# Performance work log

Measured on AMD Instinct MI355X. Metric: run time of the kernel, lower is better.

Reference implementation:

```python
import jax, jax.numpy as jnp
import numpy as np

B, D, N, MSRC, H = 4, 256, 2048, 2048, 4
DIM = D // H  # per-head dim = 64
EPS = 1e-3


def _conv1x1(W, b, z):
    # 1x1 Conv1d == per-position linear: W [out,in], z [B,in,N]
    return jnp.einsum('oc,bcn->bon', W, z) + b[None, :, None]


def setup_inputs() -> dict:
    key = jax.random.key(0)
    ks = jax.random.split(key, 20)
    s = 0.05
    x = jax.random.normal(ks[0], (B, D, N), dtype=jnp.float32)
    source = jax.random.normal(ks[1], (B, D, MSRC), dtype=jnp.float32)
    mask = (jax.random.uniform(ks[2], (B, N, MSRC)) > 0.3).astype(jnp.float32)
    Wq = jax.random.normal(ks[3], (D, D), jnp.float32) * s
    bq = jax.random.normal(ks[4], (D,), jnp.float32) * s
    Wk = jax.random.normal(ks[5], (D, D), jnp.float32) * s
    bk = jax.random.normal(ks[6], (D,), jnp.float32) * s
    Wv = jax.random.normal(ks[7], (D, D), jnp.float32) * s
    bv = jax.random.normal(ks[8], (D,), jnp.float32) * s
    Wm = jax.random.normal(ks[9], (D, D), jnp.float32) * s
    bm = jax.random.normal(ks[10], (D,), jnp.float32) * s
    W1 = jax.random.normal(ks[11], (2 * D, 2 * D), jnp.float32) * s
    b1 = jax.random.normal(ks[12], (2 * D,), jnp.float32) * s
    gamma = jnp.ones((2 * D,), jnp.float32)
    beta = jnp.zeros((2 * D,), jnp.float32)
    rmean = jax.random.normal(ks[13], (2 * D,), jnp.float32) * 0.1
    rvar = jax.random.uniform(ks[14], (2 * D,), jnp.float32) + 0.5
    W2 = jax.random.normal(ks[15], (D, 2 * D), jnp.float32) * s
    b2 = jnp.zeros((D,), jnp.float32)  # nn.init.constant_(mlp[-1].bias, 0.0)
    return dict(x=x, source=source, mask=mask, Wq=Wq, bq=bq, Wk=Wk, bk=bk,
                Wv=Wv, bv=bv, Wm=Wm, bm=bm, W1=W1, b1=b1, gamma=gamma,
                beta=beta, rmean=rmean, rvar=rvar, W2=W2, b2=b2)


def reference(x, source, mask, Wq, bq, Wk, bk, Wv, bv, Wm, bm,
              W1, b1, gamma, beta, rmean, rvar, W2, b2):
    b = x.shape[0]
    # channel dim split as (dim, heads) per torch .view(B, dim, H, -1)
    q = _conv1x1(Wq, bq, x).reshape(b, DIM, H, -1)        # [B,d,H,N]
    k = _conv1x1(Wk, bk, source).reshape(b, DIM, H, -1)   # [B,d,H,M]
    v = _conv1x1(Wv, bv, source).reshape(b, DIM, H, -1)   # [B,d,H,M]
    scores = jnp.einsum('bdhn,bdhm->bhnm', q, k) / (DIM ** 0.5)
    neg = -jnp.finfo(scores.dtype).max
    scores = jnp.where(mask[:, None, :, :] > 0, scores, neg)
    prob = jax.nn.softmax(scores, axis=-1)                # [B,H,N,M]
    msg = jnp.einsum('bhnm,bdhm->bdhn', prob, v).reshape(b, D, -1)
    message = _conv1x1(Wm, bm, msg)                       # [B,D,N]
    y = jnp.concatenate([x, message], axis=1)             # [B,2D,N]
    h = _conv1x1(W1, b1, y)
    # BatchNorm1d (eval mode, eps=1e-3)
    h = (h - rmean[None, :, None]) * jax.lax.rsqrt(rvar + EPS)[None, :, None]
    h = h * gamma[None, :, None] + beta[None, :, None]
    h = jax.nn.relu(h)
    return _conv1x1(W2, b2, h)                            # [B,D,N]
```

## Files before the change

kernel.cpp:

```cpp
#include <hip/hip_runtime.h>

constexpr int Bb = 4;
constexpr int Dd = 256;
constexpr int Nn = 2048;
constexpr int Mm = 2048;
constexpr int Hh = 4;
constexpr int D2 = 512;
constexpr int NT = Bb * Nn;

#define FMAXV 3.402823466e38f

typedef _Float16 half8 __attribute__((ext_vector_type(8)));
typedef _Float16 half4v __attribute__((ext_vector_type(4)));
typedef float f32x4 __attribute__((ext_vector_type(4)));

typedef const __attribute__((address_space(1))) void* gas_p;
typedef __attribute__((address_space(3))) void* las_p;

__device__ __forceinline__ void gload16(const void* g, void* l) {
    __builtin_amdgcn_global_load_lds((gas_p)g, (las_p)l, 16, 0, 0);
}

__global__ __launch_bounds__(256)
void prep_all_kernel(const float* __restrict__ Wq, const float* __restrict__ bq,
                     const float* __restrict__ Wk, const float* __restrict__ bk,
                     const float* __restrict__ Wv, const float* __restrict__ bv,
                     const float* __restrict__ Wm,
                     const float* __restrict__ W1, const float* __restrict__ b1,
                     const float* __restrict__ gamma, const float* __restrict__ beta,
                     const float* __restrict__ rmean, const float* __restrict__ rvar,
                     const float* __restrict__ W2, const float* __restrict__ mask,
                     const float* __restrict__ x, const float* __restrict__ source,
                     _Float16* __restrict__ Wqp, float* __restrict__ bqp,
                     _Float16* __restrict__ Wkvp, float* __restrict__ bkvp,
                     _Float16* __restrict__ Wmp,
                     _Float16* __restrict__ W1p, float* __restrict__ b1f,
                     _Float16* __restrict__ W2p,
                     unsigned long long* __restrict__ bmask,
                     _Float16* __restrict__ Yp, _Float16* __restrict__ Sp) {
    const int r = blockIdx.x, t = threadIdx.x;
    if (r < 256) {
        const int h = r >> 6, d = r & 63, so = d * Hh + h;
        Wqp[r * 256 + t] = (_Float16)Wq[so * 256 + t];
        if (t == 0) bqp[r] = bq[so];
    } else if (r < 768) {
        const int rr = r - 256, part = rr >> 8, o = rr & 255;
        const int h = o >> 6, d = o & 63, so = d * Hh + h;
        const float* Ws = part ? Wv : Wk;
        const float* bs = part ? bv : bk;
        Wkvp[rr * 256 + t] = (_Float16)Ws[so * 256 + t];
        if (t == 0) bkvp[rr] = bs[so];
    } else if (r < 1024) {
        const int o = r - 768;
        const int h = t >> 6, d = t & 63, sk = d * Hh + h;
        Wmp[o * 256 + t] = (_Float16)Wm[o * 256 + sk];
    } else if (r < 1536) {
        const int o = r - 1024;
        const float s = gamma[o] * rsqrtf(rvar[o] + 1e-3f);
        W1p[o * 512 + t]       = (_Float16)(W1[o * 512 + t] * s);
        W1p[o * 512 + t + 256] = (_Float16)(W1[o * 512 + t + 256] * s);
        if (t == 0) b1f[o] = (b1[o] - rmean[o]) * s + beta[o];
    } else if (r < 1792) {
        const int o = r - 1536;
        W2p[o * 512 + t]       = (_Float16)W2[o * 512 + t];
        W2p[o * 512 + t + 256] = (_Float16)W2[o * 512 + t + 256];
    } else if (r < 3840) {
        const int id = r - 1792;
        const int w = t >> 6, lane = t & 63;
        const int row = id * 4 + w;
        const float* mrow = mask + (size_t)row * Mm;
        unsigned long long* brow = bmask + (size_t)row * (Mm / 64);
        #pragma unroll 4
        for (int word = 0; word < Mm / 64; ++word) {
            const float v = mrow[word * 64 + lane];
            const unsigned long long bits = __ballot(v > 0.f);
            if (lane == 0) brow[word] = bits;
        }
    } else {
        __shared__ _Float16 Ts[64][72];
        const int px = r - 3840;
        const int n0 = (px & 31) * 64, c0 = ((px >> 5) & 3) * 64;
        const int z = px >> 7, b = z >> 1, which = z & 1;
        const float* src = which ? source : x;
        _Float16* dst = which ? Sp : Yp;
        const int stride = which ? 256 : 512;
        const int cl = t >> 2, np = (t & 3) * 16;
        const float* sp = src + ((size_t)b * Dd + c0 + cl) * Nn + n0 + np;
        #pragma unroll
        for (int i = 0; i < 4; ++i) {
            float4 v = *(const float4*)(sp + i * 4);
            Ts[np + i * 4 + 0][cl] = (_Float16)v.x;
            Ts[np + i * 4 + 1][cl] = (_Float16)v.y;
            Ts[np + i * 4 + 2][cl] = (_Float16)v.z;
            Ts[np + i * 4 + 3][cl] = (_Float16)v.w;
        }
        __syncthreads();
        const int nl = t >> 2, cp = (t & 3) * 16;
        half8 a0 = *(const half8*)&Ts[nl][cp];
        half8 a1 = *(const half8*)&Ts[nl][cp + 8];
        _Float16* dp = dst + ((size_t)b * Nn + n0 + nl) * stride + c0 + cp;
        *(half8*)dp = a0;
        *(half8*)(dp + 8) = a1;
    }
}

__global__ __launch_bounds__(256)
void gemm4w_kernel(const _Float16* __restrict__ A, const _Float16* __restrict__ A2,
                   const _Float16* __restrict__ W, const float* __restrict__ bias,
                   _Float16* __restrict__ dst0, _Float16* __restrict__ dst1,
                   _Float16* __restrict__ dst2, float* __restrict__ dstF,
                   int K, int sA, int sOut, int modeSel, int relu, float oscale) {
    __shared__ __align__(16) _Float16 As[2 * 128 * 64];
    __shared__ __align__(16) _Float16 Bs[2 * 64 * 64];
    __shared__ __align__(16) _Float16 Es[4][16][72];

    const int t = threadIdx.x;
    const int w = t >> 6, lane = t & 63, quad = lane >> 4, l16 = lane & 15;
    const int n0 = blockIdx.x * 128;
    const int og0 = blockIdx.y * 64;

    int mode = 0, oloc0 = og0;
    const _Float16* Ab = A;
    int sAl = sA;
    _Float16* d0 = dst0;
    float osc = oscale;
    if (modeSel == 3) {
        const int part = blockIdx.y >> 2;
        if (part == 1)      { Ab = A2; sAl = 256; d0 = dst1; oloc0 = og0 - 256; osc = 1.0f; }
        else if (part == 2) { Ab = A2; sAl = 256; mode = 1; oloc0 = og0 - 512; osc = 1.0f; }
    } else if (modeSel == 2) {
        mode = 2;
    }

    const int srow = t >> 3, sslot = t & 7;
    const int schunk = sslot ^ (srow & 7);

    f32x4 acc[2][4] = {};
    const int nk = K / 64;
    int buf = 0;

    {
        #pragma unroll
        for (int c = 0; c < 4; ++c)
            gload16(Ab + (size_t)(n0 + c * 32 + srow) * sAl + schunk * 8,
                    As + c * 2048 + t * 8);
        #pragma unroll
        for (int c = 0; c < 2; ++c)
            gload16(W + (size_t)(og0 + c * 32 + srow) * K + schunk * 8,
                    Bs + c * 2048 + t * 8);
        __asm__ volatile("s_waitcnt vmcnt(0)" ::: "memory");
        __syncthreads();
    }

    #pragma unroll 1
    for (int kt = 0; kt < nk; ++kt) {
        if (kt + 1 < nk) {
            const int k0 = (kt + 1) * 64, nb = buf ^ 1;
            #pragma unroll
            for (int c = 0; c < 4; ++c)
                gload16(Ab + (size_t)(n0 + c * 32 + srow) * sAl + k0 + schunk * 8,
                        As + nb * 8192 + c * 2048 + t * 8);
            #pragma unroll
            for (int c = 0; c < 2; ++c)
                gload16(W + (size_t)(og0 + c * 32 + srow) * K + k0 + schunk * 8,
                        Bs + nb * 4096 + c * 2048 + t * 8);
        }
        #pragma unroll
        for (int ks = 0; ks < 2; ++ks) {
            const int csw = ((ks * 4 + quad) ^ (l16 & 7)) * 8;
            half8 af[2], bf[4];
            #pragma unroll
            for (int i = 0; i < 2; ++i)
                af[i] = *(const half8*)&As[buf * 8192 + (w * 32 + i * 16 + l16) * 64 + csw];
            #pragma unroll
            for (int j = 0; j < 4; ++j)
                bf[j] = *(const half8*)&Bs[buf * 4096 + (j * 16 + l16) * 64 + csw];
            #pragma unroll
            for (int i = 0; i < 2; ++i)
                #pragma unroll
                for (int j = 0; j < 4; ++j)
                    acc[i][j] = __builtin_amdgcn_mfma_f32_16x16x32_f16(af[i], bf[j], acc[i][j], 0, 0, 0);
        }
        if (kt + 1 < nk) {
            __asm__ volatile("s_waitcnt vmcnt(0)" ::: "memory");
            __syncthreads();
            buf ^= 1;
        }
    }

    float bcol[4];
    #pragma unroll
    for (int j = 0; j < 4; ++j) bcol[j] = bias[og0 + j * 16 + l16];

    if (mode == 0) {
        #pragma unroll
        for (int i = 0; i < 2; ++i) {
            #pragma unroll
            for (int j = 0; j < 4; ++j)
                #pragma unroll
                for (int reg = 0; reg < 4; ++reg) {
                    float v = (acc[i][j][reg] + bcol[j]) * osc;
                    if (relu) v = fmaxf(v, 0.f);
                    Es[w][quad * 4 + reg][j * 16 + l16] = (_Float16)v;
                }
            __asm__ volatile("s_waitcnt lgkmcnt(0)" ::: "memory");
            const int row = lane & 15, oseg = (lane >> 4) * 16;
            half8 e0 = *(const half8*)&Es[w][row][oseg];
            half8 e1 = *(const half8*)&Es[w][row][oseg + 8];
            _Float16* dp = d0 + (size_t)(n0 + w * 32 + i * 16 + row) * sOut + oloc0 + oseg;
            *(half8*)dp = e0;
            *(half8*)(dp + 8) = e1;
            __asm__ volatile("s_waitcnt lgkmcnt(0)" ::: "memory");
        }
    } else if (mode == 1) {
        #pragma unroll
        for (int i = 0; i < 2; ++i) {
            const int ng = n0 + w * 32 + i * 16 + quad * 4;
            const int bidx = ng >> 11, m0 = ng & 2047;
            #pragma unroll
            for (int j = 0; j < 4; ++j) {
                const int o = oloc0 + j * 16 + l16;
                half4v pv;
                #pragma unroll
                for (int reg = 0; reg < 4; ++reg) pv[reg] = (_Float16)(acc[i][j][reg] + bcol[j]);
                *(half4v*)(dst2 + ((size_t)bidx * 256 + o) * (size_t)Mm + m0) = pv;
            }
        }
    } else {
        #pragma unroll
        for (int i = 0; i < 2; ++i) {
            const int ng = n0 + w * 32 + i * 16 + quad * 4;
            const int bidx = ng >> 11, m0 = ng & 2047;
            #pragma unroll
            for (int j = 0; j < 4; ++j) {
                const int o = og0 + j * 16 + l16;
                f32x4 v;
                #pragma unroll
                for (int reg = 0; reg < 4; ++reg) v[reg] = acc[i][j][reg] + bcol[j];
                *(f32x4*)(dstF + ((size_t)bidx * 256 + o) * (size_t)Nn + m0) = v;
            }
        }
    }
}

__global__ __launch_bounds__(256)
void attn_mfma_kernel(const _Float16* __restrict__ Qp, const _Float16* __restrict__ Kp,
                      const _Float16* __restrict__ Vt,
                      const unsigned int* __restrict__ bmask,
                      _Float16* __restrict__ Oa, _Float16* __restrict__ Ob,
                      float* __restrict__ La, float* __restrict__ Lb) {
    __shared__ __align__(16) _Float16 Ks[64][72];
    __shared__ __align__(16) _Float16 Vs[64][72];
    __shared__ __align__(16) _Float16 Ps[4][16][72];

    const int id = blockIdx.x;
    const int xcd = id & 7, loc = id >> 3;
    const int bh = xcd * 2 + (loc >> 6);
    const int sub = loc & 63;
    const int mhalf = sub & 1;
    const int n0 = (sub >> 1) * 64;
    const int b = bh >> 2, h = bh & 3;

    const int t = threadIdx.x;
    const int w = t >> 6, lane = t & 63, quad = lane >> 4, l16 = lane & 15;

    const _Float16* qp = Qp + ((size_t)b * Nn + n0 + w * 16 + l16) * 256 + h * 64 + quad * 8;
    const half8 qa0 = *(const half8*)(qp);
    const half8 qa1 = *(const half8*)(qp + 32);

    const _Float16* Kstg = Kp + (size_t)b * Nn * 256 + h * 64;
    const _Float16* Vstg = Vt + ((size_t)b * 256 + h * 64) * (size_t)Mm;
    const int sr = t >> 2, sc = (t & 3) * 16;

    const unsigned int* bmBase = bmask + ((size_t)b * Nn + n0 + w * 16 + quad * 4) * (Mm / 32);

    _Float16* Od = mhalf ? Ob : Oa;
    float* Ld = mhalf ? Lb : La;
    const int mbeg = mhalf * (Mm / 2);

    float lo[4] = {0.f, 0.f, 0.f, 0.f};
    f32x4 O[4] = {};

    half8 sk0, sk1, sv0, sv1;
    auto stage_load = [&](int m0) {
        const _Float16* ks = Kstg + (size_t)(m0 + sr) * 256 + sc;
        sk0 = *(const half8*)(ks);
        sk1 = *(const half8*)(ks + 8);
        const _Float16* vs = Vstg + (size_t)sr * Mm + m0 + sc;
        sv0 = *(const half8*)(vs);
        sv1 = *(const half8*)(vs + 8);
    };
    auto stage_write = [&]() {
        *(half8*)&Ks[sr][sc]     = sk0;
        *(half8*)&Ks[sr][sc + 8] = sk1;
        *(half8*)&Vs[sr][sc]     = sv0;
        *(half8*)&Vs[sr][sc + 8] = sv1;
    };

    stage_load(mbeg);
    stage_write();
    __syncthreads();

    #pragma unroll 1
    for (int it = 0; it < (Mm / 2) / 64; ++it) {
        const int m0 = mbeg + it * 64;
        if (it < (Mm / 2) / 64 - 1) stage_load(m0 + 64);

        uint2 bmv[4];
        #pragma unroll
        for (int reg = 0; reg < 4; ++reg)
            bmv[reg] = *(const uint2*)(bmBase + (size_t)reg * (Mm / 32) + (m0 >> 5));

        f32x4 S[4];
        #pragma unroll
        for (int mt = 0; mt < 4; ++mt) {
            half8 k0 = *(const half8*)&Ks[mt * 16 + l16][quad * 8];
            half8 k1 = *(const half8*)&Ks[mt * 16 + l16][32 + quad * 8];
            f32x4 z = {0.f, 0.f, 0.f, 0.f};
            z = __builtin_amdgcn_mfma_f32_16x16x32_f16(qa0, k0, z, 0, 0, 0);
            z = __builtin_amdgcn_mfma_f32_16x16x32_f16(qa1, k1, z, 0, 0, 0);
            S[mt] = z;
        }

        float p[4][4];
        #pragma unroll
        for (int reg = 0; reg < 4; ++reg) {
            const unsigned losh = bmv[reg].x >> l16;
            const unsigned hish = bmv[reg].y >> l16;
            p[0][reg] = (losh & 1u)         ? __expf(S[0][reg]) : 0.f;
            p[1][reg] = ((losh >> 16) & 1u) ? __expf(S[1][reg]) : 0.f;
            p[2][reg] = (hish & 1u)         ? __expf(S[2][reg]) : 0.f;
            p[3][reg] = ((hish >> 16) & 1u) ? __expf(S[3][reg]) : 0.f;
        }
        #pragma unroll
        for (int reg = 0; reg < 4; ++reg)
            lo[reg] += (p[0][reg] + p[1][reg]) + (p[2][reg] + p[3][reg]);

        #pragma unroll
        for (int mt = 0; mt < 4; ++mt)
            #pragma unroll
            for (int reg = 0; reg < 4; ++reg)
                Ps[w][quad * 4 + reg][mt * 16 + l16] = (_Float16)p[mt][reg];
        __asm__ volatile("s_waitcnt lgkmcnt(0)" ::: "memory");
        half8 pa0 = *(const half8*)&Ps[w][l16][quad * 8];
        half8 pa1 = *(const half8*)&Ps[w][l16][32 + quad * 8];

        #pragma unroll
        for (int dt = 0; dt < 4; ++dt) {
            half8 v0 = *(const half8*)&Vs[dt * 16 + l16][quad * 8];
            half8 v1 = *(const half8*)&Vs[dt * 16 + l16][32 + quad * 8];
            O[dt] = __builtin_amdgcn_mfma_f32_16x16x32_f16(pa0, v0, O[dt], 0, 0, 0);
            O[dt] = __builtin_amdgcn_mfma_f32_16x16x32_f16(pa1, v1, O[dt], 0, 0, 0);
        }

        if (it < (Mm / 2) / 64 - 1) {
            __syncthreads();
            stage_write();
            __syncthreads();
        }
    }

    #pragma unroll
    for (int reg = 0; reg < 4; ++reg) {
        float s = lo[reg];
        s += __shfl_xor(s, 1);
        s += __shfl_xor(s, 2);
        s += __shfl_xor(s, 4);
        s += __shfl_xor(s, 8);
        lo[reg] = s;
    }

    _Float16* op = Od + ((size_t)b * Nn + n0 + w * 16 + quad * 4) * 256 + h * 64 + l16;
    #pragma unroll
    for (int reg = 0; reg < 4; ++reg)
        #pragma unroll
        for (int dt = 0; dt < 4; ++dt)
            op[(size_t)reg * 256 + dt * 16] = (_Float16)(O[dt][reg] * 0.0625f);
    if (l16 == 0) {
        #pragma unroll
        for (int reg = 0; reg < 4; ++reg)
            Ld[((size_t)b * Nn + n0 + w * 16 + quad * 4 + reg) * 4 + h] = lo[reg] * 0.0625f;
    }
}

__global__ __launch_bounds__(256)
void combine_kernel(const _Float16* __restrict__ Oa, const _Float16* __restrict__ Ob,
                    const float* __restrict__ La, const float* __restrict__ Lb,
                    _Float16* __restrict__ out) {
    const int gid = blockIdx.x * 256 + threadIdx.x;
    const int row = gid >> 5, chunk = gid & 31;
    const int h = chunk >> 3;
    const float L = La[row * 4 + h] + Lb[row * 4 + h];
    const float inv = 1.0f / L;
    half8 a = *(const half8*)(Oa + (size_t)row * 256 + chunk * 8);
    half8 c = *(const half8*)(Ob + (size_t)row * 256 + chunk * 8);
    half8 o;
    #pragma unroll
    for (int k = 0; k < 8; ++k)
        o[k] = (_Float16)(((float)a[k] + (float)c[k]) * inv);
    *(half8*)(out + (size_t)row * 256 + chunk * 8) = o;
}

extern "C" void kernel_launch(void* const* d_in, const int* in_sizes, int n_in,
                              void* d_out, int out_size, void* d_ws, size_t ws_size,
                              hipStream_t stream) {
    const float* x      = (const float*)d_in[0];
    const float* source = (const float*)d_in[1];
    const float* mask   = (const float*)d_in[2];
    const float* Wq = (const float*)d_in[3];
    const float* bq = (const float*)d_in[4];
    const float* Wk = (const float*)d_in[5];
    const float* bk = (const float*)d_in[6];
    const float* Wv = (const float*)d_in[7];
    const float* bv = (const float*)d_in[8];
    const float* Wm = (const float*)d_in[9];
    const float* bm = (const float*)d_in[10];
    const float* W1 = (const float*)d_in[11];
    const float* b1 = (const float*)d_in[12];
    const float* gamma = (const float*)d_in[13];
    const float* beta  = (const float*)d_in[14];
    const float* rmean = (const float*)d_in[15];
    const float* rvar  = (const float*)d_in[16];
    const float* W2 = (const float*)d_in[17];
    const float* b2 = (const float*)d_in[18];
    float* outp = (float*)d_out;

    char* wsb = (char*)d_ws;
    _Float16* Yp   = (_Float16*)wsb;
    _Float16* Sp   = (_Float16*)(wsb + (8u << 20));
    _Float16* Qp   = (_Float16*)(wsb + (12u << 20));
    _Float16* Kp   = (_Float16*)(wsb + (16u << 20));
    _Float16* Vt   = (_Float16*)(wsb + (20u << 20));
    _Float16* msgp = (_Float16*)(wsb + (24u << 20));
    _Float16* Hp   = (_Float16*)(wsb + (28u << 20));
    unsigned long long* bmask = (unsigned long long*)(wsb + (28u << 20));
    _Float16* Ob = (_Float16*)(wsb + (30u << 20));
    float* La = (float*)(wsb + (34u << 20));
    float* Lb = (float*)(wsb + (34u << 20) + (128u << 10));
    char* wp = wsb + (36u << 20);
    _Float16* Wqp  = (_Float16*)wp;            wp += 256 * 256 * 2;
    _Float16* Wkvp = (_Float16*)wp;            wp += 512 * 256 * 2;
    _Float16* Wmp  = (_Float16*)wp;            wp += 256 * 256 * 2;
    _Float16* W1p  = (_Float16*)wp;            wp += 512 * 512 * 2;
    _Float16* W2p  = (_Float16*)wp;            wp += 256 * 512 * 2;
    float* bqp  = (float*)wp;                  wp += 256 * 4;
    float* bkvp = (float*)wp;                  wp += 512 * 4;
    float* b1f  = (float*)wp;                  wp += 512 * 4;

    prep_all_kernel<<<4864, 256, 0, stream>>>(
        Wq, bq, Wk, bk, Wv, bv, Wm, W1, b1, gamma, beta, rmean, rvar, W2, mask,
        x, source, Wqp, bqp, Wkvp, bkvp, Wmp, W1p, b1f, W2p, bmask, Yp, Sp);

    gemm4w_kernel<<<dim3(NT / 128, 12), 256, 0, stream>>>(
        Yp, Sp, Wqp, bqp, Qp, Kp, Vt, nullptr, 256, 512, 256, 3, 0, 0.125f);

    attn_mfma_kernel<<<1024, 256, 0, stream>>>(Qp, Kp, Vt,
                                               (const unsigned int*)bmask,
                                               msgp, Ob, La, Lb);

    combine_kernel<<<1024, 256, 0, stream>>>(msgp, Ob, La, Lb, Sp);

    gemm4w_kernel<<<dim3(NT / 128, 4), 256, 0, stream>>>(
        Sp, nullptr, Wmp, bm, Yp + 256, nullptr, nullptr, nullptr, 256, 256, 512, 0, 0, 1.0f);
    gemm4w_kernel<<<dim3(NT / 128, 8), 256, 0, stream>>>(
        Yp, nullptr, W1p, b1f, Hp, nullptr, nullptr, nullptr, 512, 512, 512, 0, 1, 1.0f);
    gemm4w_kernel<<<dim3(NT / 128, 4), 256, 0, stream>>>(
        Hp, nullptr, W2p, b2, nullptr, nullptr, nullptr, outp, 512, 512, 0, 2, 0, 1.0f);
}
```

Measured before the change: 237.7 us.

## Fuse attention combine, merge projection, and MLP into one kernel

Replaces the combine kernel and three separate GEMM launches with one kernel per 16-row tile. The tile merges the two attention halves, applies the Wm projection, W1 with ReLU, and W2, keeping intermediates in LDS so the msg and hidden activations never round-trip through global memory. Weights are read directly from global/L2 with no LDS staging. Only 512 blocks run and each uses a 16-row tile, so weight reuse per block is low and occupancy may be limited.

```diff
diff --git a/kernel.cpp b/kernel.cpp
--- a/kernel.cpp
+++ b/kernel.cpp
@@ -383,22 +383,126 @@
     }
 }
 
+template<int NJ>
+__device__ __forceinline__ void mm_stage(const _Float16* As, int sAl,
+                                         const _Float16* W, int K,
+                                         int oc0, int l16, int quad,
+                                         f32x4 (&acc)[NJ]) {
+    const _Float16* bRow[NJ];
+    #pragma unroll
+    for (int j = 0; j < NJ; ++j)
+        bRow[j] = W + (size_t)(oc0 + j * 16 + l16) * K + quad * 8;
+    const _Float16* aBase = As + l16 * sAl + quad * 8;
+
+    half8 b0[NJ], b1[NJ], a0, a1;
+    #pragma unroll
+    for (int j = 0; j < NJ; ++j) b0[j] = *(const half8*)(bRow[j]);
+    a0 = *(const half8*)(aBase);
+
+    #pragma unroll 1
+    for (int k0 = 0; k0 < K; k0 += 64) {
+        #pragma unroll
+        for (int j = 0; j < NJ; ++j) b1[j] = *(const half8*)(bRow[j] + k0 + 32);
+        a1 = *(const half8*)(aBase + k0 + 32);
+        #pragma unroll
+        for (int j = 0; j < NJ; ++j)
+            acc[j] = __builtin_amdgcn_mfma_f32_16x16x32_f16(a0, b0[j], acc[j], 0, 0, 0);
+        if (k0 + 64 < K) {
+            #pragma unroll
+            for (int j = 0; j < NJ; ++j) b0[j] = *(const half8*)(bRow[j] + k0 + 64);
+            a0 = *(const half8*)(aBase + k0 + 64);
+        }
+        #pragma unroll
+        for (int j = 0; j < NJ; ++j)
+            acc[j] = __builtin_amdgcn_mfma_f32_16x16x32_f16(a1, b1[j], acc[j], 0, 0, 0);
+    }
+}
+
 __global__ __launch_bounds__(256)
-void combine_kernel(const _Float16* __restrict__ Oa, const _Float16* __restrict__ Ob,
-                    const float* __restrict__ La, const float* __restrict__ Lb,
-                    _Float16* __restrict__ out) {
-    const int gid = blockIdx.x * 256 + threadIdx.x;
-    const int row = gid >> 5, chunk = gid & 31;
-    const int h = chunk >> 3;
-    const float L = La[row * 4 + h] + Lb[row * 4 + h];
-    const float inv = 1.0f / L;
-    half8 a = *(const half8*)(Oa + (size_t)row * 256 + chunk * 8);
-    half8 c = *(const half8*)(Ob + (size_t)row * 256 + chunk * 8);
-    half8 o;
-    #pragma unroll
-    for (int k = 0; k < 8; ++k)
-        o[k] = (_Float16)(((float)a[k] + (float)c[k]) * inv);
-    *(half8*)(out + (size_t)row * 256 + chunk * 8) = o;
+void fused_mlp_kernel(const _Float16* __restrict__ Yp,
+                      const _Float16* __restrict__ Oa, const _Float16* __restrict__ Ob,
+                      const float* __restrict__ La, const float* __restrict__ Lb,
+                      const _Float16* __restrict__ Wmp, const float* __restrict__ bm,
+                      const _Float16* __restrict__ W1p, const float* __restrict__ b1f,
+                      const _Float16* __restrict__ W2p, const float* __restrict__ b2,
+                      float* __restrict__ outp) {
+    __shared__ __align__(16) _Float16 y[16][520];
+    __shared__ __align__(16) _Float16 hbuf[16 * 520];
+
+    const int t = threadIdx.x;
+    const int w = t >> 6, lane = t & 63, quad = lane >> 4, l16 = lane & 15;
+    const int n0 = blockIdx.x * 16;
+
+    {
+        const int row = t >> 4, ch = t & 15, col0 = ch * 16, hh = ch >> 2;
+        const size_t gr = (size_t)(n0 + row);
+        const _Float16* xs = Yp + gr * 512 + col0;
+        *(half8*)&y[row][col0]     = *(const half8*)(xs);
+        *(half8*)&y[row][col0 + 8] = *(const half8*)(xs + 8);
+        const float inv = 1.0f / (La[gr * 4 + hh] + Lb[gr * 4 + hh]);
+        half8 oa0 = *(const half8*)(Oa + gr * 256 + col0);
+        half8 oa1 = *(const half8*)(Oa + gr * 256 + col0 + 8);
+        half8 ob0 = *(const half8*)(Ob + gr * 256 + col0);
+        half8 ob1 = *(const half8*)(Ob + gr * 256 + col0 + 8);
+        half8 m0, m1;
+        #pragma unroll
+        for (int k = 0; k < 8; ++k) {
+            m0[k] = (_Float16)(((float)oa0[k] + (float)ob0[k]) * inv);
+            m1[k] = (_Float16)(((float)oa1[k] + (float)ob1[k]) * inv);
+        }
+        *(half8*)&hbuf[row * 264 + col0]     = m0;
+        *(half8*)&hbuf[row * 264 + col0 + 8] = m1;
+    }
+    __syncthreads();
+
+    {
+        const int oc0 = w * 64;
+        f32x4 acc[4] = {};
+        mm_stage<4>(hbuf, 264, Wmp, 256, oc0, l16, quad, acc);
+        float bcol[4];
+        #pragma unroll
+        for (int j = 0; j < 4; ++j) bcol[j] = bm[oc0 + j * 16 + l16];
+        #pragma unroll
+        for (int j = 0; j < 4; ++j)
+            #pragma unroll
+            for (int reg = 0; reg < 4; ++reg)
+                y[quad * 4 + reg][256 + oc0 + j * 16 + l16] =
+                    (_Float16)(acc[j][reg] + bcol[j]);
+    }
+    __syncthreads();
+
+    {
+        const int oc0 = w * 128;
+        f32x4 acc[8] = {};
+        mm_stage<8>(&y[0][0], 520, W1p, 512, oc0, l16, quad, acc);
+        float bcol[8];
+        #pragma unroll
+        for (int j = 0; j < 8; ++j) bcol[j] = b1f[oc0 + j * 16 + l16];
+        #pragma unroll
+        for (int j = 0; j < 8; ++j)
+            #pragma unroll
+            for (int reg = 0; reg < 4; ++reg)
+                hbuf[(quad * 4 + reg) * 520 + oc0 + j * 16 + l16] =
+                    (_Float16)fmaxf(acc[j][reg] + bcol[j], 0.f);
+    }
+    __syncthreads();
+
+    {
+        const int oc0 = w * 64;
+        f32x4 acc[4] = {};
+        mm_stage<4>(hbuf, 520, W2p, 512, oc0, l16, quad, acc);
+        const int m0 = (n0 & 2047) + quad * 4;
+        const int bidx = n0 >> 11;
+        #pragma unroll
+        for (int j = 0; j < 4; ++j) {
+            const int o = oc0 + j * 16 + l16;
+            const float bc = b2[o];
+            f32x4 v;
+            #pragma unroll
+            for (int reg = 0; reg < 4; ++reg) v[reg] = acc[j][reg] + bc;
+            *(f32x4*)(outp + ((size_t)bidx * 256 + o) * (size_t)Nn + m0) = v;
+        }
+    }
 }
 
 extern "C" void kernel_launch(void* const* d_in, const int* in_sizes, int n_in,
@@ -431,8 +535,7 @@
     _Float16* Qp   = (_Float16*)(wsb + (12u << 20));
     _Float16* Kp   = (_Float16*)(wsb + (16u << 20));
     _Float16* Vt   = (_Float16*)(wsb + (20u << 20));
-    _Float16* msgp = (_Float16*)(wsb + (24u << 20));
-    _Float16* Hp   = (_Float16*)(wsb + (28u << 20));
+    _Float16* Oa   = (_Float16*)(wsb + (24u << 20));
     unsigned long long* bmask = (unsigned long long*)(wsb + (28u << 20));
     _Float16* Ob = (_Float16*)(wsb + (30u << 20));
     float* La = (float*)(wsb + (34u << 20));
@@ -456,14 +559,8 @@
 
     attn_mfma_kernel<<<1024, 256, 0, stream>>>(Qp, Kp, Vt,
                                                (const unsigned int*)bmask,
-                                               msgp, Ob, La, Lb);
-
-    combine_kernel<<<1024, 256, 0, stream>>>(msgp, Ob, La, Lb, Sp);
-
-    gemm4w_kernel<<<dim3(NT / 128, 4), 256, 0, stream>>>(
-        Sp, nullptr, Wmp, bm, Yp + 256, nullptr, nullptr, nullptr, 256, 256, 512, 0, 0, 1.0f);
-    gemm4w_kernel<<<dim3(NT / 128, 8), 256, 0, stream>>>(
-        Yp, nullptr, W1p, b1f, Hp, nullptr, nullptr, nullptr, 512, 512, 512, 0, 1, 1.0f);
-    gemm4w_kernel<<<dim3(NT / 128, 4), 256, 0, stream>>>(
-        Hp, nullptr, W2p, b2, nullptr, nullptr, nullptr, outp, 512, 512, 0, 2, 0, 1.0f);
-}
+                                               Oa, Ob, La, Lb);
+
+    fused_mlp_kernel<<<512, 256, 0, stream>>>(
+        Yp, Oa, Ob, La, Lb, Wmp, bm, W1p, b1f, W2p, b2, outp);
+}
```

Result: slower. 257.9 us (+8.5%).

## Fuse split-attention combine into message GEMM and stage transposed epilogues in LDS

Applied to the files above, without the earlier changes.

Removes the separate combine kernel by having a new message-projection GEMM load both partial attention outputs and their normalizers, merge them in registers, and write the merged tile into LDS as its A operand. The transposed-output epilogues (V layout and the final fp32 output) now go through swizzled LDS scratch so that global writes become contiguous 16-element rows instead of scattered 4-element chunks. The epilogue scratch now reuses the A-tile buffer, which cuts shared memory per block. The fused GEMM reads twice the A data and does a division per row chunk, and its A path uses register staging rather than async LDS loads.

```diff
diff --git a/kernel.cpp b/kernel.cpp
--- a/kernel.cpp
+++ b/kernel.cpp
@@ -112,7 +112,6 @@
                    int K, int sA, int sOut, int modeSel, int relu, float oscale) {
     __shared__ __align__(16) _Float16 As[2 * 128 * 64];
     __shared__ __align__(16) _Float16 Bs[2 * 64 * 64];
-    __shared__ __align__(16) _Float16 Es[4][16][72];
 
     const int t = threadIdx.x;
     const int w = t >> 6, lane = t & 63, quad = lane >> 4, l16 = lane & 15;
@@ -193,6 +192,7 @@
     for (int j = 0; j < 4; ++j) bcol[j] = bias[og0 + j * 16 + l16];
 
     if (mode == 0) {
+        _Float16* Escr = As + w * 2048;
         #pragma unroll
         for (int i = 0; i < 2; ++i) {
             #pragma unroll
@@ -201,12 +201,12 @@
                 for (int reg = 0; reg < 4; ++reg) {
                     float v = (acc[i][j][reg] + bcol[j]) * osc;
                     if (relu) v = fmaxf(v, 0.f);
-                    Es[w][quad * 4 + reg][j * 16 + l16] = (_Float16)v;
+                    Escr[(quad * 4 + reg) * 72 + j * 16 + l16] = (_Float16)v;
                 }
             __asm__ volatile("s_waitcnt lgkmcnt(0)" ::: "memory");
             const int row = lane & 15, oseg = (lane >> 4) * 16;
-            half8 e0 = *(const half8*)&Es[w][row][oseg];
-            half8 e1 = *(const half8*)&Es[w][row][oseg + 8];
+            half8 e0 = *(const half8*)&Escr[row * 72 + oseg];
+            half8 e1 = *(const half8*)&Escr[row * 72 + oseg + 8];
             _Float16* dp = d0 + (size_t)(n0 + w * 32 + i * 16 + row) * sOut + oloc0 + oseg;
             *(half8*)dp = e0;
             *(half8*)(dp + 8) = e1;
@@ -214,31 +214,57 @@
         }
     } else if (mode == 1) {
         #pragma unroll
-        for (int i = 0; i < 2; ++i) {
-            const int ng = n0 + w * 32 + i * 16 + quad * 4;
-            const int bidx = ng >> 11, m0 = ng & 2047;
+        for (int i = 0; i < 2; ++i)
             #pragma unroll
             for (int j = 0; j < 4; ++j) {
-                const int o = oloc0 + j * 16 + l16;
+                const int c = j * 16 + l16;
+                const int mloc = w * 32 + i * 16 + quad * 4;
+                const int sw = l16 * 8;
                 half4v pv;
                 #pragma unroll
-                for (int reg = 0; reg < 4; ++reg) pv[reg] = (_Float16)(acc[i][j][reg] + bcol[j]);
-                *(half4v*)(dst2 + ((size_t)bidx * 256 + o) * (size_t)Mm + m0) = pv;
+                for (int reg = 0; reg < 4; ++reg)
+                    pv[reg] = (_Float16)(acc[i][j][reg] + bcol[j]);
+                *(half4v*)&As[c * 128 + (mloc ^ sw)] = pv;
             }
+        __syncthreads();
+        const int n0m = n0 & 2047, bidx = n0 >> 11;
+        #pragma unroll
+        for (int r = 0; r < 2; ++r) {
+            const int c = (t >> 3) + r * 32;
+            const int mch = (t & 7) * 16;
+            const int sw = (c & 15) * 8;
+            half8 v0 = *(const half8*)&As[c * 128 + (mch ^ sw)];
+            half8 v1 = *(const half8*)&As[c * 128 + ((mch + 8) ^ sw)];
+            _Float16* dp = dst2 + ((size_t)bidx * 256 + oloc0 + c) * (size_t)Mm + n0m + mch;
+            *(half8*)dp = v0;
+            *(half8*)(dp + 8) = v1;
         }
     } else {
-        #pragma unroll
-        for (int i = 0; i < 2; ++i) {
-            const int ng = n0 + w * 32 + i * 16 + quad * 4;
-            const int bidx = ng >> 11, m0 = ng & 2047;
+        __syncthreads();
+        float* scr = (float*)As;
+        #pragma unroll
+        for (int i = 0; i < 2; ++i)
             #pragma unroll
             for (int j = 0; j < 4; ++j) {
-                const int o = og0 + j * 16 + l16;
+                const int c = j * 16 + l16;
+                const int mloc = w * 32 + i * 16 + quad * 4;
+                const int sw = (c & 7) * 4;
                 f32x4 v;
                 #pragma unroll
                 for (int reg = 0; reg < 4; ++reg) v[reg] = acc[i][j][reg] + bcol[j];
-                *(f32x4*)(dstF + ((size_t)bidx * 256 + o) * (size_t)Nn + m0) = v;
+                *(f32x4*)&scr[c * 128 + (mloc ^ sw)] = v;
             }
+        __syncthreads();
+        const int n0m = n0 & 2047, bidx = n0 >> 11;
+        #pragma unroll
+        for (int r = 0; r < 2; ++r) {
+            const int c = (t >> 3) + r * 32;
+            const int mch = (t & 7) * 16;
+            const int sw = (c & 7) * 4;
+            float* dp = dstF + ((size_t)bidx * 256 + og0 + c) * (size_t)Nn + n0m + mch;
+            #pragma unroll
+            for (int k = 0; k < 4; ++k)
+                *(f32x4*)(dp + k * 4) = *(const f32x4*)&scr[c * 128 + ((mch + k * 4) ^ sw)];
         }
     }
 }
@@ -384,21 +410,112 @@
 }
 
 __global__ __launch_bounds__(256)
-void combine_kernel(const _Float16* __restrict__ Oa, const _Float16* __restrict__ Ob,
-                    const float* __restrict__ La, const float* __restrict__ Lb,
-                    _Float16* __restrict__ out) {
-    const int gid = blockIdx.x * 256 + threadIdx.x;
-    const int row = gid >> 5, chunk = gid & 31;
-    const int h = chunk >> 3;
-    const float L = La[row * 4 + h] + Lb[row * 4 + h];
-    const float inv = 1.0f / L;
-    half8 a = *(const half8*)(Oa + (size_t)row * 256 + chunk * 8);
-    half8 c = *(const half8*)(Ob + (size_t)row * 256 + chunk * 8);
-    half8 o;
+void gemm_msg_kernel(const _Float16* __restrict__ Oa, const _Float16* __restrict__ Ob,
+                     const float* __restrict__ La, const float* __restrict__ Lb,
+                     const _Float16* __restrict__ W, const float* __restrict__ bias,
+                     _Float16* __restrict__ dst) {
+    __shared__ __align__(16) _Float16 As[2 * 128 * 64];
+    __shared__ __align__(16) _Float16 Bs[2 * 64 * 64];
+
+    const int t = threadIdx.x;
+    const int w = t >> 6, lane = t & 63, quad = lane >> 4, l16 = lane & 15;
+    const int n0 = blockIdx.x * 128;
+    const int og0 = blockIdx.y * 64;
+    const int srow = t >> 3, sslot = t & 7;
+    const int schunk = sslot ^ (srow & 7);
+    constexpr int K = 256;
+
+    f32x4 acc[2][4] = {};
+
+    half8 oa[4], ob[4];
+    float inv[4];
+
+    auto loadA = [&](int k0) {
+        const int h = k0 >> 6;
+        #pragma unroll
+        for (int c = 0; c < 4; ++c) {
+            const size_t row = (size_t)(n0 + c * 32 + srow);
+            oa[c] = *(const half8*)(Oa + row * 256 + k0 + schunk * 8);
+            ob[c] = *(const half8*)(Ob + row * 256 + k0 + schunk * 8);
+            inv[c] = 1.0f / (La[row * 4 + h] + Lb[row * 4 + h]);
+        }
+    };
+    auto writeA = [&](int nb) {
+        #pragma unroll
+        for (int c = 0; c < 4; ++c) {
+            half8 m;
+            #pragma unroll
+            for (int k = 0; k < 8; ++k)
+                m[k] = (_Float16)(((float)oa[c][k] + (float)ob[c][k]) * inv[c]);
+            *(half8*)&As[nb * 8192 + c * 2048 + t * 8] = m;
+        }
+    };
+    auto loadB = [&](int k0, int nb) {
+        #pragma unroll
+        for (int c = 0; c < 2; ++c)
+            gload16(W + (size_t)(og0 + c * 32 + srow) * K + k0 + schunk * 8,
+                    Bs + nb * 4096 + c * 2048 + t * 8);
+    };
+
+    loadA(0);
+    loadB(0, 0);
+    writeA(0);
+    __asm__ volatile("s_waitcnt vmcnt(0)" ::: "memory");
+    __syncthreads();
+
+    int buf = 0;
+    #pragma unroll 1
+    for (int kt = 0; kt < 4; ++kt) {
+        if (kt < 3) {
+            loadA((kt + 1) * 64);
+            loadB((kt + 1) * 64, buf ^ 1);
+        }
+        #pragma unroll
+        for (int ks = 0; ks < 2; ++ks) {
+            const int csw = ((ks * 4 + quad) ^ (l16 & 7)) * 8;
+            half8 af[2], bf[4];
+            #pragma unroll
+            for (int i = 0; i < 2; ++i)
+                af[i] = *(const half8*)&As[buf * 8192 + (w * 32 + i * 16 + l16) * 64 + csw];
+            #pragma unroll
+            for (int j = 0; j < 4; ++j)
+                bf[j] = *(const half8*)&Bs[buf * 4096 + (j * 16 + l16) * 64 + csw];
+            #pragma unroll
+            for (int i = 0; i < 2; ++i)
+                #pragma unroll
+                for (int j = 0; j < 4; ++j)
+                    acc[i][j] = __builtin_amdgcn_mfma_f32_16x16x32_f16(af[i], bf[j], acc[i][j], 0, 0, 0);
+        }
+        if (kt < 3) {
+            writeA(buf ^ 1);
+            __asm__ volatile("s_waitcnt vmcnt(0)" ::: "memory");
+            __syncthreads();
+            buf ^= 1;
+        }
+    }
+
+    float bcol[4];
     #pragma unroll
-    for (int k = 0; k < 8; ++k)
-        o[k] = (_Float16)(((float)a[k] + (float)c[k]) * inv);
-    *(half8*)(out + (size_t)row * 256 + chunk * 8) = o;
+    for (int j = 0; j < 4; ++j) bcol[j] = bias[og0 + j * 16 + l16];
+
+    _Float16* Escr = As + w * 2048;
+    #pragma unroll
+    for (int i = 0; i < 2; ++i) {
+        #pragma unroll
+        for (int j = 0; j < 4; ++j)
+            #pragma unroll
+            for (int reg = 0; reg < 4; ++reg)
+                Escr[(quad * 4 + reg) * 72 + j * 16 + l16] =
+                    (_Float16)(acc[i][j][reg] + bcol[j]);
+        __asm__ volatile("s_waitcnt lgkmcnt(0)" ::: "memory");
+        const int row = lane & 15, oseg = (lane >> 4) * 16;
+        half8 e0 = *(const half8*)&Escr[row * 72 + oseg];
+        half8 e1 = *(const half8*)&Escr[row * 72 + oseg + 8];
+        _Float16* dp = dst + (size_t)(n0 + w * 32 + i * 16 + row) * 512 + og0 + oseg;
+        *(half8*)dp = e0;
+        *(half8*)(dp + 8) = e1;
+        __asm__ volatile("s_waitcnt lgkmcnt(0)" ::: "memory");
+    }
 }
 
 extern "C" void kernel_launch(void* const* d_in, const int* in_sizes, int n_in,
@@ -431,7 +548,7 @@
     _Float16* Qp   = (_Float16*)(wsb + (12u << 20));
     _Float16* Kp   = (_Float16*)(wsb + (16u << 20));
     _Float16* Vt   = (_Float16*)(wsb + (20u << 20));
-    _Float16* msgp = (_Float16*)(wsb + (24u << 20));
+    _Float16* Oa   = (_Float16*)(wsb + (24u << 20));
     _Float16* Hp   = (_Float16*)(wsb + (28u << 20));
     unsigned long long* bmask = (unsigned long long*)(wsb + (28u << 20));
     _Float16* Ob = (_Float16*)(wsb + (30u << 20));
@@ -456,12 +573,11 @@
 
     attn_mfma_kernel<<<1024, 256, 0, stream>>>(Qp, Kp, Vt,
                                                (const unsigned int*)bmask,
-                                               msgp, Ob, La, Lb);
-
-    combine_kernel<<<1024, 256, 0, stream>>>(msgp, Ob, La, Lb, Sp);
-
-    gemm4w_kernel<<<dim3(NT / 128, 4), 256, 0, stream>>>(
-        Sp, nullptr, Wmp, bm, Yp + 256, nullptr, nullptr, nullptr, 256, 256, 512, 0, 0, 1.0f);
+                                               Oa, Ob, La, Lb);
+
+    gemm_msg_kernel<<<dim3(NT / 128, 4), 256, 0, stream>>>(
+        Oa, Ob, La, Lb, Wmp, bm, Yp + 256);
+
     gemm4w_kernel<<<dim3(NT / 128, 8), 256, 0, stream>>>(
         Yp, nullptr, W1p, b1f, Hp, nullptr, nullptr, nullptr, 512, 512, 512, 0, 1, 1.0f);
     gemm4w_kernel<<<dim3(NT / 128, 4), 256, 0, stream>>>(
```

Result: no change. 233.3 us (-1.9%).
